# Kernel tuning notes

Measured on AMD Instinct MI355X. Metric: run time of the kernel, lower is better.

## Reference

```python
import jax, jax.numpy as jnp
import numpy as np

LN_EPS = 1e-5

def layer_norm(x, gamma, beta):
    mu = jnp.mean(x, axis=-1, keepdims=True)
    var = jnp.mean(jnp.square(x - mu), axis=-1, keepdims=True)
    return (x - mu) * jax.lax.rsqrt(var + LN_EPS) * gamma + beta

def setup_inputs() -> dict:
    key = jax.random.key(0)
    ks = jax.random.split(key, 10)
    B, C, N = 8, 256, 4096
    s = 1.0 / np.sqrt(C)
    inp = {
        "x": jax.random.normal(ks[0], (B, C, N), dtype=jnp.float32),
        "W_qkv": jax.random.uniform(ks[1], (C, C), jnp.float32, -s, s),            # Linear(dim, dim, bias=False)
        "W_mlp": jax.random.uniform(ks[2], (2 * C, 2 * C), jnp.float32, -0.5 * s, 0.5 * s),
        "b_mlp": jax.random.uniform(ks[3], (2 * C,), jnp.float32, -0.5 * s, 0.5 * s),
        "g1": jnp.ones((4 * C,), jnp.float32),
        "beta1": jnp.zeros((4 * C,), jnp.float32),
        "W_res": jax.random.uniform(ks[4], (C, 4 * C), jnp.float32, -0.25 * s, 0.25 * s),  # Linear(4*dim, dim, bias=False)
        "g2": jnp.ones((C,), jnp.float32),
        "beta2": jnp.zeros((C,), jnp.float32),
    }
    return inp

def reference(x, W_qkv, W_mlp, b_mlp, g1, beta1, W_res, g2, beta2):
    # x: (B, C, N) channels-first -> (B, N, C)
    NITER = 2  # niter_heads
    x = jnp.swapaxes(x, 1, 2)
    x = x @ W_qkv.T                                   # shared_qkv, (B, N, C)
    v = jax.lax.stop_gradient(x)                      # x.clone().detach()
    for _ in range(NITER):
        # first_context = x^T @ v : (B, C, C)
        ctx = jnp.einsum('bnc,bnd->bcd', x, v)
        out = jax.nn.softmax(x, axis=-1) @ ctx        # (B, N, C)
        cat1 = jnp.concatenate([out, v], axis=-1)     # (B, N, 2C)
        mlp = jax.nn.relu(cat1 @ W_mlp.T + b_mlp)     # (B, N, 2C)
        cat2 = jnp.concatenate([cat1, mlp], axis=-1)  # (B, N, 4C)
        # dropout layers are identity in eval mode
        v = layer_norm(cat2, g1, beta1) @ W_res.T + x # residual_mlp + skip
        v = layer_norm(x + v, g2, beta2)
    return jnp.swapaxes(v, 1, 2)                      # back to (B, C, N)
```

## Files before the change

### kernel.cpp

```cpp
#include <hip/hip_runtime.h>
#include <cstdint>
#include <cstddef>


using u16 = unsigned short;
using short8 = __attribute__((ext_vector_type(8))) short;
using bf16x8 = __attribute__((ext_vector_type(8))) __bf16;
using f32x4  = __attribute__((ext_vector_type(4))) float;
using i32x4  = __attribute__((ext_vector_type(4))) int;
using u16x4  = __attribute__((ext_vector_type(4))) u16;
using u16x8  = __attribute__((ext_vector_type(8))) u16;

__device__ __forceinline__ float b2f(u16 u) {
    union { unsigned u32; float f; } c; c.u32 = ((unsigned)u) << 16; return c.f;
}
__device__ __forceinline__ u16 f2b(float f) {
    union { float f; unsigned u; } c; c.f = f;
    unsigned r = c.u + 0x7FFFu + ((c.u >> 16) & 1u);
    return (u16)(r >> 16);
}
__device__ __forceinline__ void cvt(u16 a,  u16& o)   { o = a; }
__device__ __forceinline__ void cvt(float a, u16& o)  { o = f2b(a); }
__device__ __forceinline__ void cvt(float a, float& o){ o = a; }
__device__ __forceinline__ void cvt(u16 a,  float& o) { o = b2f(a); }

__device__ __forceinline__ void glds16(const u16* g, short* l) {
    __builtin_amdgcn_global_load_lds(
        (const __attribute__((address_space(1))) void*)g,
        (__attribute__((address_space(3))) void*)l, 16, 0, 0);
}

template<int MODE, int TRF>
__global__ __launch_bounds__(512)
void gemm_bt(const u16* __restrict__ A, const u16* __restrict__ A2,
             const u16* __restrict__ A3,
             int lda, int lda2, int lda3, int kSplit,
             const u16* __restrict__ B, int ldb, long strA, long strB,
             int statStride, int kChunk, int nKsplit,
             float* __restrict__ outF, u16* __restrict__ outB,
             long sOF, long sOB, int ldo,
             const u16* __restrict__ Xres,
             const float* __restrict__ bias,
             const float2* __restrict__ stats,
             const float* __restrict__ g, const float* __restrict__ be)
{
    __shared__ short lsA[128 * 64];
    __shared__ short lsB[128 * 64];

    const int bz    = blockIdx.z;
    const int batch = bz / nKsplit;
    const int ks    = bz - batch * nKsplit;
    const u16* Ab = A + (size_t)batch * strA;
    const u16* Bb = B + (size_t)batch * strB;
    const int colBase = blockIdx.x * 128;
    const int rowBase = blockIdx.y * 128;
    const int k0 = ks * kChunk;
    const int k1 = k0 + kChunk;

    const int t    = threadIdx.x;
    const int sRow = t >> 3;
    const int sKl  = (t & 7) << 3;
    const int sKg  = (((t & 7) ^ (sRow & 7)) << 3);

    const int lane = t & 63;
    const int w    = t >> 6;
    const int wr   = (w >> 1) * 32;
    const int wc   = (w & 1) * 64;
    const int mrow = lane & 15;
    const int q    = lane >> 4;

    short* ldA0 = &lsA[w * 512];
    short* ldA1 = &lsA[4096 + w * 512];
    short* ldB0 = &lsB[w * 512];
    short* ldB1 = &lsB[4096 + w * 512];

    float2 st0 = {0.f, 0.f}, st1 = {0.f, 0.f};
    if (TRF == 1) {
        const int sb = batch * statStride + rowBase;
        const float2 t0 = stats[sb + sRow];
        const float2 t1 = stats[sb + sRow + 64];
        st0 = make_float2(0.f, 1.f / t0.y);
        st1 = make_float2(0.f, 1.f / t1.y);
    }

    auto aPtr = [&](int rloc, int kn) -> const u16* {
        const int arow = rowBase + rloc + sRow;
        if (TRF == 2) {
            if (kn < 256)      return A  + (size_t)arow * lda  + kn + sKg;
            else if (kn < 512) return A2 + (size_t)arow * lda2 + (kn - 256) + sKg;
            else               return A3 + (size_t)arow * lda3 + (kn - 512) + sKg;
        } else if (TRF == 3) {
            if (kn < kSplit)   return Ab + (size_t)arow * lda + kn + sKg;
            return A2 + (size_t)arow * lda2 + (kn - kSplit) + sKg;
        }
        return Ab + (size_t)arow * lda + kn + sKg;
    };
    auto loadX = [&](int rloc, int kn, float2 st) -> i32x4 {
        const int arow = rowBase + rloc + sRow;
        i32x4 raw = *(const i32x4*)(Ab + (size_t)arow * lda + kn + sKg);
        short8 h = __builtin_bit_cast(short8, raw);
        short8 o;
#pragma unroll
        for (int i = 0; i < 8; i++) {
            float v = b2f((u16)h[i]);
            v = __expf(v - st.x) * st.y;
            o[i] = (short)f2b(v);
        }
        return __builtin_bit_cast(i32x4, o);
    };

    const f32x4 fzero = {0.f, 0.f, 0.f, 0.f};
    f32x4 acc[2][4];
#pragma unroll
    for (int i = 0; i < 2; i++)
#pragma unroll
        for (int j = 0; j < 4; j++) acc[i][j] = fzero;

    const u16* pB0 = Bb + (size_t)(colBase + sRow) * ldb + sKg;
    const u16* pB1 = pB0 + (size_t)64 * ldb;
    const u16* pA0 = nullptr; const u16* pA1 = nullptr;
    if (TRF == 0) {
        pA0 = Ab + (size_t)(rowBase + sRow) * lda + sKg;
        pA1 = pA0 + (size_t)64 * lda;
    }

    const int rsw = mrow & 7;
    const int kc0 = (((0 * 4 + q) ^ rsw) << 3);
    const int kc1 = (((1 * 4 + q) ^ rsw) << 3);

    i32x4 a0, a1;
    if (TRF == 1) {
        a0 = loadX(0,  k0, st0);
        a1 = loadX(64, k0, st1);
    }

    for (int kk = k0; kk < k1; kk += 64) {
        if (TRF == 1) {
            *(i32x4*)&lsA[sRow * 64 + sKl]        = a0;
            *(i32x4*)&lsA[(sRow + 64) * 64 + sKl] = a1;
        } else if (TRF == 0) {
            glds16(pA0 + kk, ldA0);
            glds16(pA1 + kk, ldA1);
        } else {
            glds16(aPtr(0,  kk), ldA0);
            glds16(aPtr(64, kk), ldA1);
        }
        glds16(pB0 + kk, ldB0);
        glds16(pB1 + kk, ldB1);
        __syncthreads();
        const int kn = kk + 64;
        if (TRF == 1 && kn < k1) {
            a0 = loadX(0,  kn, st0);
            a1 = loadX(64, kn, st1);
        }
#pragma unroll
        for (int h = 0; h < 2; h++) {
            const int kc = h ? kc1 : kc0;
            bf16x8 af[2], bfr[4];
#pragma unroll
            for (int mi = 0; mi < 2; mi++)
                af[mi] = __builtin_bit_cast(bf16x8,
                    *(const short8*)&lsA[(wr + mi * 16 + mrow) * 64 + kc]);
#pragma unroll
            for (int ni = 0; ni < 4; ni++)
                bfr[ni] = __builtin_bit_cast(bf16x8,
                    *(const short8*)&lsB[(wc + ni * 16 + mrow) * 64 + kc]);
#pragma unroll
            for (int mi = 0; mi < 2; mi++)
#pragma unroll
                for (int ni = 0; ni < 4; ni++)
                    acc[mi][ni] = __builtin_amdgcn_mfma_f32_16x16x32_bf16(
                        af[mi], bfr[ni], acc[mi][ni], 0, 0, 0);
        }
        __syncthreads();
    }

    if (MODE == 5) {
        u16* XT = const_cast<u16*>(Xres);
        float2* sm = const_cast<float2*>(stats);
        float rsum[2][4] = {{0.f,0.f,0.f,0.f},{0.f,0.f,0.f,0.f}};
#pragma unroll
        for (int mi = 0; mi < 2; mi++) {
#pragma unroll
            for (int ni = 0; ni < 4; ni++) {
                const int col  = colBase + wc + ni * 16 + mrow;
                const int row0 = rowBase + wr + mi * 16 + q * 4;
                u16x4 hv;
#pragma unroll
                for (int r = 0; r < 4; r++) {
                    const u16 h = f2b(acc[mi][ni][r]);
                    hv[r] = h;
                    outB[(size_t)(row0 + r) * ldo + col] = h;
                    rsum[mi][r] += __expf(b2f(h));
                }
                *(u16x4*)(XT + (size_t)(row0 >> 12) * 1048576
                             + (size_t)col * 4096 + (row0 & 4095)) = hv;
            }
        }
#pragma unroll
        for (int mi = 0; mi < 2; mi++)
#pragma unroll
            for (int r = 0; r < 4; r++) {
                float s = rsum[mi][r];
                s += __shfl_xor(s, 1); s += __shfl_xor(s, 2);
                s += __shfl_xor(s, 4); s += __shfl_xor(s, 8);
                if (mrow == 0)
                    atomicAdd(&sm[rowBase + wr + mi * 16 + q * 4 + r].y, s);
            }
        return;
    }

#pragma unroll
    for (int mi = 0; mi < 2; mi++) {
#pragma unroll
        for (int ni = 0; ni < 4; ni++) {
            const int col = colBase + wc + ni * 16 + mrow;
#pragma unroll
            for (int r = 0; r < 4; r++) {
                const int row = rowBase + wr + mi * 16 + q * 4 + r;
                float v = acc[mi][ni][r];
                if (MODE == 0) {
                    outB[(size_t)batch * sOB + (size_t)row * ldo + col] = f2b(v);
                } else if (MODE == 1) {
                    outF[((size_t)batch * nKsplit + ks) * sOF
                         + (size_t)row * ldo + col] = v;
                } else if (MODE == 3) {
                    v += bias[col];
                    v = v > 0.f ? v : 0.f;
                    outB[(size_t)row * ldo + col] = f2b(v);
                } else if (MODE == 4) {
                    const float2 ln = stats[row];
                    v = ln.y * (v - ln.x * g[col]) + be[col]
                        + 2.f * b2f(Xres[(size_t)row * 256 + col]);
                    outB[(size_t)row * ldo + col] = f2b(v);
                }
            }
        }
    }
}

template<typename TIN, typename TOUT>
__global__ __launch_bounds__(256)
void transpose_k(const TIN* __restrict__ in, TOUT* __restrict__ out,
                 int R, int Cc, long sIn, long sOut)
{
    __shared__ TOUT tile[32][33];
    const int b = blockIdx.z;
    const TIN* ib = in + (size_t)b * sIn;
    TOUT* ob = out + (size_t)b * sOut;
    const int c0 = blockIdx.x * 32, r0 = blockIdx.y * 32;
    const int tx = threadIdx.x & 31, ty = threadIdx.x >> 5;
#pragma unroll
    for (int i = 0; i < 32; i += 8)
        cvt(ib[(size_t)(r0 + ty + i) * Cc + c0 + tx], tile[ty + i][tx]);
    __syncthreads();
#pragma unroll
    for (int i = 0; i < 32; i += 8)
        ob[(size_t)(c0 + ty + i) * R + r0 + tx] = tile[tx][ty + i];
}

__global__ __launch_bounds__(256)
void zerosm_k(float2* __restrict__ p)
{
    p[blockIdx.x * 256 + threadIdx.x] = make_float2(0.f, 0.f);
}

__global__ __launch_bounds__(256)
void stats1024_k(const u16* __restrict__ OUT, const u16* __restrict__ V,
                 const u16* __restrict__ MLPo, float2* __restrict__ st)
{
    const int wave = threadIdx.x >> 6, lane = threadIdx.x & 63;
    const size_t row = (size_t)blockIdx.x * 4 + wave;
    const int c = lane * 16;
    const u16* src;
    if (c < 256)       src = OUT  + row * 256 + c;
    else if (c < 512)  src = V    + row * 256 + (c - 256);
    else               src = MLPo + row * 512 + (c - 512);
    short8 r0 = *(const short8*)(src);
    short8 r1 = *(const short8*)(src + 8);
    float s = 0.f, s2 = 0.f;
#pragma unroll
    for (int i = 0; i < 8; i++) {
        const float a = b2f((u16)r0[i]), b = b2f((u16)r1[i]);
        s += a + b; s2 += a * a + b * b;
    }
    for (int o = 32; o > 0; o >>= 1) { s += __shfl_xor(s, o); s2 += __shfl_xor(s2, o); }
    const float mean = s * (1.f / 1024.f);
    const float var  = s2 * (1.f / 1024.f) - mean * mean;
    if (lane == 0) st[row] = make_float2(mean, rsqrtf(var + 1e-5f));
}

template<typename OUTT, bool WRITE_VB>
__global__ __launch_bounds__(256)
void ln256t_k(const u16* __restrict__ Tb, const float* __restrict__ g,
              const float* __restrict__ be, u16* __restrict__ Vb,
              OUTT* __restrict__ outT)
{
    constexpr int STRIDE = (sizeof(OUTT) == 2) ? 266 : 261;
    __shared__ OUTT tile[32 * STRIDE];
    const int wid = threadIdx.x >> 6, lane = threadIdx.x & 63;
    const int bx = blockIdx.x;
    const size_t r0 = (size_t)bx * 32;
    const int b  = bx >> 7;
    const int n0 = (bx & 127) * 32;

#pragma unroll
    for (int j = 0; j < 8; j++) {
        const int lr = wid * 8 + j;
        const size_t row = r0 + lr;
        const u16x4 tb = *(const u16x4*)(Tb + row * 256 + lane * 4);
        const float x0 = b2f(tb.x), x1 = b2f(tb.y), x2 = b2f(tb.z), x3 = b2f(tb.w);
        float s  = x0 + x1 + x2 + x3;
        float s2 = x0 * x0 + x1 * x1 + x2 * x2 + x3 * x3;
        for (int o = 32; o > 0; o >>= 1) { s += __shfl_xor(s, o); s2 += __shfl_xor(s2, o); }
        const float mean = s * (1.f / 256.f);
        const float var  = s2 * (1.f / 256.f) - mean * mean;
        const float rstd = rsqrtf(var + 1e-5f);
        const int c = lane * 4;
        float4 ov = { (x0 - mean) * rstd * g[c + 0] + be[c + 0],
                      (x1 - mean) * rstd * g[c + 1] + be[c + 1],
                      (x2 - mean) * rstd * g[c + 2] + be[c + 2],
                      (x3 - mean) * rstd * g[c + 3] + be[c + 3] };
        if (WRITE_VB) {
            u16x4 vb = { f2b(ov.x), f2b(ov.y), f2b(ov.z), f2b(ov.w) };
            *(u16x4*)(Vb + row * 256 + c) = vb;
        }
        OUTT* tl = &tile[lr * STRIDE + c];
        cvt(ov.x, tl[0]); cvt(ov.y, tl[1]); cvt(ov.z, tl[2]); cvt(ov.w, tl[3]);
    }
    __syncthreads();

    const int c = threadIdx.x;
    OUTT* dst = outT + ((size_t)b * 256 + c) * 4096 + n0;
    if (sizeof(OUTT) == 2) {
#pragma unroll
        for (int k = 0; k < 4; k++) {
            u16x8 v;
#pragma unroll
            for (int i = 0; i < 8; i++) v[i] = *(const u16*)&tile[(k * 8 + i) * STRIDE + c];
            *(u16x8*)((u16*)dst + k * 8) = v;
        }
    } else {
#pragma unroll
        for (int k = 0; k < 8; k++) {
            float4 v;
            v.x = *(const float*)&tile[(k * 4 + 0) * STRIDE + c];
            v.y = *(const float*)&tile[(k * 4 + 1) * STRIDE + c];
            v.z = *(const float*)&tile[(k * 4 + 2) * STRIDE + c];
            v.w = *(const float*)&tile[(k * 4 + 3) * STRIDE + c];
            *(float4*)((float*)dst + k * 4) = v;
        }
    }
}

__global__ __launch_bounds__(256)
void ctxreduce_k(const float* __restrict__ ctxp, u16* __restrict__ ctxb)
{
    const int i = blockIdx.x * 256 + threadIdx.x;
    const int batch  = i >> 14;
    const int within = i & 16383;
    const float4* src = (const float4*)ctxp + (size_t)batch * 16 * 16384 + within;
    float4 s = {0.f, 0.f, 0.f, 0.f};
#pragma unroll
    for (int ks = 0; ks < 16; ks++) {
        const float4 v = src[(size_t)ks * 16384];
        s.x += v.x; s.y += v.y; s.z += v.z; s.w += v.w;
    }
    u16x4 o = { f2b(s.x), f2b(s.y), f2b(s.z), f2b(s.w) };
    ((u16x4*)ctxb)[i] = o;
}

__global__ __launch_bounds__(256)
void wconv_k(const float* __restrict__ Wq, const float* __restrict__ Wm,
             u16* __restrict__ oq, u16* __restrict__ om)
{
    const int i = blockIdx.x * 256 + threadIdx.x;
    const float* src; u16* dst; int j;
    if (i < 16384) { src = Wq; dst = oq; j = i; }
    else           { src = Wm; dst = om; j = i - 16384; }
    const float4 v = ((const float4*)src)[j];
    u16x4 o = { f2b(v.x), f2b(v.y), f2b(v.z), f2b(v.w) };
    ((u16x4*)dst)[j] = o;
}

__global__ __launch_bounds__(256)
void wresprep_k(const float* __restrict__ Wres, const float* __restrict__ g1,
                const float* __restrict__ be1, u16* __restrict__ Wr_b,
                float* __restrict__ sg, float* __restrict__ br)
{
    const int wv = threadIdx.x >> 6, lane = threadIdx.x & 63;
    const int row = blockIdx.x * 4 + wv;
    const float* src = Wres + (size_t)row * 1024;
    float s = 0.f, b = 0.f;
#pragma unroll
    for (int j = 0; j < 4; j++) {
        const int c = j * 256 + lane * 4;
        const float4 w  = *(const float4*)(src + c);
        const float4 gg = *(const float4*)(g1 + c);
        const float4 bb = *(const float4*)(be1 + c);
        const float4 wg = { w.x * gg.x, w.y * gg.y, w.z * gg.z, w.w * gg.w };
        u16x4 o = { f2b(wg.x), f2b(wg.y), f2b(wg.z), f2b(wg.w) };
        *(u16x4*)(Wr_b + (size_t)row * 1024 + c) = o;
        s += wg.x + wg.y + wg.z + wg.w;
        b += w.x * bb.x + w.y * bb.y + w.z * bb.z + w.w * bb.w;
    }
    for (int o = 32; o > 0; o >>= 1) { s += __shfl_xor(s, o); b += __shfl_xor(b, o); }
    if (lane == 0) { sg[row] = s; br[row] = b; }
}

extern "C" void kernel_launch(void* const* d_in, const int* in_sizes, int n_in,
                              void* d_out, int out_size, void* d_ws, size_t ws_size,
                              hipStream_t stream)
{
    (void)in_sizes; (void)n_in; (void)out_size; (void)ws_size;
    const float* x    = (const float*)d_in[0];
    const float* Wqkv = (const float*)d_in[1];
    const float* Wmlp = (const float*)d_in[2];
    const float* bmlp = (const float*)d_in[3];
    const float* g1   = (const float*)d_in[4];
    const float* be1  = (const float*)d_in[5];
    const float* Wres = (const float*)d_in[6];
    const float* g2   = (const float*)d_in[7];
    const float* be2  = (const float*)d_in[8];

    char* ws = (char*)d_ws;
    u16*    Xb   = (u16*)ws;    ws += (size_t)16777216;
    u16*    XT   = (u16*)ws;    ws += (size_t)16777216;
    u16*    Vb   = (u16*)ws;    ws += (size_t)16777216;
    u16*    VT2  = (u16*)ws;    ws += (size_t)16777216;
    u16*    OUT  = (u16*)ws;    ws += (size_t)16777216;
    u16*    MLPo = (u16*)ws;    ws += (size_t)33554432;
    u16*    Tb   = (u16*)ws;    ws += (size_t)16777216;
    float*  ctxp = (float*)ws;  ws += (size_t)33554432;
    u16*    ctxb = (u16*)ws;    ws += (size_t)1048576;
    float2* smst = (float2*)ws; ws += (size_t)262144;
    float2* lnst = (float2*)ws; ws += (size_t)262144;
    u16*    Wq_b = (u16*)ws;    ws += (size_t)131072;
    u16*    Wm_b = (u16*)ws;    ws += (size_t)524288;
    u16*    Wr_b = (u16*)ws;    ws += (size_t)524288;
    float*  sg   = (float*)ws;  ws += (size_t)1024;
    float*  br   = (float*)ws;  ws += (size_t)1024;
    u16*    xt   = MLPo;

    wconv_k<<<dim3(320), 256, 0, stream>>>(Wqkv, Wmlp, Wq_b, Wm_b);
    wresprep_k<<<dim3(64), 256, 0, stream>>>(Wres, g1, be1, Wr_b, sg, br);
    zerosm_k<<<dim3(128), 256, 0, stream>>>(smst);

    transpose_k<float, u16><<<dim3(128, 8, 8), 256, 0, stream>>>(
        x, xt, 256, 4096, 256L * 4096, 4096L * 256);

    gemm_bt<5, 0><<<dim3(2, 256, 1), 512, 0, stream>>>(
        xt, nullptr, nullptr, 256, 0, 0, 0, Wq_b, 256, 0, 0, 0, 256, 1,
        nullptr, Xb, 0, 0, 256, XT, nullptr, smst, nullptr, nullptr);

    const u16* VTcur = XT;
    const u16* Vcur  = Xb;

    for (int it = 0; it < 2; ++it) {
        gemm_bt<1, 0><<<dim3(2, 2, 128), 512, 0, stream>>>(
            VTcur, nullptr, nullptr, 4096, 0, 0, 0, XT, 4096,
            1048576, 1048576, 0, 256, 16,
            ctxp, nullptr, 65536, 0, 256, nullptr, nullptr, nullptr, nullptr, nullptr);
        ctxreduce_k<<<dim3(512), 256, 0, stream>>>(ctxp, ctxb);

        gemm_bt<0, 1><<<dim3(2, 32, 8), 512, 0, stream>>>(
            Xb, nullptr, nullptr, 256, 0, 0, 0, ctxb, 256,
            1048576, 65536, 4096, 256, 1,
            nullptr, OUT, 0, 1048576, 256, nullptr, nullptr, smst, nullptr, nullptr);

        gemm_bt<3, 3><<<dim3(4, 256, 1), 512, 0, stream>>>(
            OUT, Vcur, nullptr, 256, 256, 0, 256, Wm_b, 512, 0, 0, 0, 512, 1,
            nullptr, MLPo, 0, 0, 512, nullptr, bmlp, nullptr, nullptr, nullptr);

        stats1024_k<<<dim3(8192), 256, 0, stream>>>(OUT, Vcur, MLPo, lnst);

        gemm_bt<4, 2><<<dim3(2, 256, 1), 512, 0, stream>>>(
            OUT, Vcur, MLPo, 256, 256, 512, 0, Wr_b, 1024, 0, 0, 0, 1024, 1,
            nullptr, Tb, 0, 0, 256, Xb, nullptr, lnst, sg, br);

        if (it == 0) {
            ln256t_k<u16, true><<<dim3(1024), 256, 0, stream>>>(
                Tb, g2, be2, Vb, VT2);
            VTcur = VT2;
            Vcur  = Vb;
        } else {
            ln256t_k<float, false><<<dim3(1024), 256, 0, stream>>>(
                Tb, g2, be2, nullptr, (float*)d_out);
        }
    }
}
```

Baseline: 355.4 us.

## Fuse LayerNorm-1024 statistics into GEMM epilogues and precompute softmax operand

Drops the separate stats1024 pass that re-read OUT, V and MLP outputs. Row sum and sum-of-squares are now accumulated with atomics in the out-GEMM and MLP-GEMM epilogues, V stats come from the LN256 kernel or a new pre-pass, and the residual GEMM derives mean and rstd itself. Softmax(x) is also materialised once as a bf16 buffer so the out-GEMM uses a plain epilogue. The cost is extra atomics, a zeroing step folded into ctxreduce, and an extra 16 MB buffer plus one pre-pass kernel.

```diff
diff --git a/kernel.cpp b/kernel.cpp
--- a/kernel.cpp
+++ b/kernel.cpp
@@ -210,6 +210,85 @@
         return;
     }
 
+    if (MODE == 6 || MODE == 7) {
+        float2* om = const_cast<float2*>(stats);
+        float ss[2][4]  = {{0.f,0.f,0.f,0.f},{0.f,0.f,0.f,0.f}};
+        float ss2[2][4] = {{0.f,0.f,0.f,0.f},{0.f,0.f,0.f,0.f}};
+#pragma unroll
+        for (int mi = 0; mi < 2; mi++) {
+#pragma unroll
+            for (int ni = 0; ni < 4; ni++) {
+                const int col = colBase + wc + ni * 16 + mrow;
+#pragma unroll
+                for (int r = 0; r < 4; r++) {
+                    const int row = rowBase + wr + mi * 16 + q * 4 + r;
+                    float v = acc[mi][ni][r];
+                    if (MODE == 7) {
+                        v += bias[col];
+                        v = v > 0.f ? v : 0.f;
+                    }
+                    const u16 h = f2b(v);
+                    outB[(size_t)batch * sOB + (size_t)row * ldo + col] = h;
+                    const float uf = b2f(h);
+                    ss[mi][r]  += uf;
+                    ss2[mi][r] += uf * uf;
+                }
+            }
+        }
+#pragma unroll
+        for (int mi = 0; mi < 2; mi++)
+#pragma unroll
+            for (int r = 0; r < 4; r++) {
+                float s  = ss[mi][r], s2 = ss2[mi][r];
+                s  += __shfl_xor(s, 1);  s  += __shfl_xor(s, 2);
+                s  += __shfl_xor(s, 4);  s  += __shfl_xor(s, 8);
+                s2 += __shfl_xor(s2, 1); s2 += __shfl_xor(s2, 2);
+                s2 += __shfl_xor(s2, 4); s2 += __shfl_xor(s2, 8);
+                if (mrow == 0) {
+                    const int grow = batch * statStride
+                                   + rowBase + wr + mi * 16 + q * 4 + r;
+                    atomicAdd(&om[grow].x, s);
+                    atomicAdd(&om[grow].y, s2);
+                }
+            }
+        return;
+    }
+
+    if (MODE == 4) {
+        const float2* om = (const float2*)bias;
+        float mean_[2][4], rstd_[2][4];
+#pragma unroll
+        for (int mi = 0; mi < 2; mi++)
+#pragma unroll
+            for (int r = 0; r < 4; r++) {
+                const int row = rowBase + wr + mi * 16 + q * 4 + r;
+                const float2 vs = stats[row];
+                const float2 os = om[row];
+                const float s  = vs.x + os.x;
+                const float s2 = vs.y + os.y;
+                const float mean = s * (1.f / 1024.f);
+                const float var  = s2 * (1.f / 1024.f) - mean * mean;
+                mean_[mi][r] = mean;
+                rstd_[mi][r] = rsqrtf(var + 1e-5f);
+            }
+#pragma unroll
+        for (int mi = 0; mi < 2; mi++) {
+#pragma unroll
+            for (int ni = 0; ni < 4; ni++) {
+                const int col = colBase + wc + ni * 16 + mrow;
+#pragma unroll
+                for (int r = 0; r < 4; r++) {
+                    const int row = rowBase + wr + mi * 16 + q * 4 + r;
+                    float v = acc[mi][ni][r];
+                    v = rstd_[mi][r] * (v - mean_[mi][r] * g[col]) + be[col]
+                        + 2.f * b2f(Xres[(size_t)row * 256 + col]);
+                    outB[(size_t)row * ldo + col] = f2b(v);
+                }
+            }
+        }
+        return;
+    }
+
 #pragma unroll
     for (int mi = 0; mi < 2; mi++) {
 #pragma unroll
@@ -228,11 +307,6 @@
                     v += bias[col];
                     v = v > 0.f ? v : 0.f;
                     outB[(size_t)row * ldo + col] = f2b(v);
-                } else if (MODE == 4) {
-                    const float2 ln = stats[row];
-                    v = ln.y * (v - ln.x * g[col]) + be[col]
-                        + 2.f * b2f(Xres[(size_t)row * 256 + col]);
-                    outB[(size_t)row * ldo + col] = f2b(v);
                 }
             }
         }
@@ -266,35 +340,28 @@
 }
 
 __global__ __launch_bounds__(256)
-void stats1024_k(const u16* __restrict__ OUT, const u16* __restrict__ V,
-                 const u16* __restrict__ MLPo, float2* __restrict__ st)
+void sxb_k(const u16* __restrict__ Xb, const float2* __restrict__ smst,
+           u16* __restrict__ SXb, float2* __restrict__ vstat)
 {
     const int wave = threadIdx.x >> 6, lane = threadIdx.x & 63;
     const size_t row = (size_t)blockIdx.x * 4 + wave;
-    const int c = lane * 16;
-    const u16* src;
-    if (c < 256)       src = OUT  + row * 256 + c;
-    else if (c < 512)  src = V    + row * 256 + (c - 256);
-    else               src = MLPo + row * 512 + (c - 512);
-    short8 r0 = *(const short8*)(src);
-    short8 r1 = *(const short8*)(src + 8);
-    float s = 0.f, s2 = 0.f;
-#pragma unroll
-    for (int i = 0; i < 8; i++) {
-        const float a = b2f((u16)r0[i]), b = b2f((u16)r1[i]);
-        s += a + b; s2 += a * a + b * b;
-    }
-    for (int o = 32; o > 0; o >>= 1) { s += __shfl_xor(s, o); s2 += __shfl_xor(s2, o); }
-    const float mean = s * (1.f / 1024.f);
-    const float var  = s2 * (1.f / 1024.f) - mean * mean;
-    if (lane == 0) st[row] = make_float2(mean, rsqrtf(var + 1e-5f));
+    const u16x4 xb = *(const u16x4*)(Xb + row * 256 + lane * 4);
+    const float rs = 1.f / smst[row].y;
+    const float x0 = b2f(xb.x), x1 = b2f(xb.y), x2 = b2f(xb.z), x3 = b2f(xb.w);
+    u16x4 o = { f2b(__expf(x0) * rs), f2b(__expf(x1) * rs),
+                f2b(__expf(x2) * rs), f2b(__expf(x3) * rs) };
+    *(u16x4*)(SXb + row * 256 + lane * 4) = o;
+    float s  = x0 + x1 + x2 + x3;
+    float s2 = x0 * x0 + x1 * x1 + x2 * x2 + x3 * x3;
+    for (int d = 32; d > 0; d >>= 1) { s += __shfl_xor(s, d); s2 += __shfl_xor(s2, d); }
+    if (lane == 0) vstat[row] = make_float2(s, s2);
 }
 
 template<typename OUTT, bool WRITE_VB>
 __global__ __launch_bounds__(256)
 void ln256t_k(const u16* __restrict__ Tb, const float* __restrict__ g,
               const float* __restrict__ be, u16* __restrict__ Vb,
-              OUTT* __restrict__ outT)
+              OUTT* __restrict__ outT, float2* __restrict__ vstat)
 {
     constexpr int STRIDE = (sizeof(OUTT) == 2) ? 266 : 261;
     __shared__ OUTT tile[32 * STRIDE];
@@ -324,6 +391,12 @@
         if (WRITE_VB) {
             u16x4 vb = { f2b(ov.x), f2b(ov.y), f2b(ov.z), f2b(ov.w) };
             *(u16x4*)(Vb + row * 256 + c) = vb;
+            const float u0 = b2f(vb.x), u1 = b2f(vb.y),
+                        u2 = b2f(vb.z), u3 = b2f(vb.w);
+            float vs  = u0 + u1 + u2 + u3;
+            float vs2 = u0 * u0 + u1 * u1 + u2 * u2 + u3 * u3;
+            for (int o = 32; o > 0; o >>= 1) { vs += __shfl_xor(vs, o); vs2 += __shfl_xor(vs2, o); }
+            if (lane == 0) vstat[row] = make_float2(vs, vs2);
         }
         OUTT* tl = &tile[lr * STRIDE + c];
         cvt(ov.x, tl[0]); cvt(ov.y, tl[1]); cvt(ov.z, tl[2]); cvt(ov.w, tl[3]);
@@ -354,9 +427,11 @@
 }
 
 __global__ __launch_bounds__(256)
-void ctxreduce_k(const float* __restrict__ ctxp, u16* __restrict__ ctxb)
+void ctxreduce_k(const float* __restrict__ ctxp, u16* __restrict__ ctxb,
+                 float2* __restrict__ om)
 {
     const int i = blockIdx.x * 256 + threadIdx.x;
+    if (i < 32768) om[i] = make_float2(0.f, 0.f);
     const int batch  = i >> 14;
     const int within = i & 16383;
     const float4* src = (const float4*)ctxp + (size_t)batch * 16 * 16384 + within;
@@ -426,6 +501,7 @@
     char* ws = (char*)d_ws;
     u16*    Xb   = (u16*)ws;    ws += (size_t)16777216;
     u16*    XT   = (u16*)ws;    ws += (size_t)16777216;
+    u16*    SXb  = (u16*)ws;    ws += (size_t)16777216;
     u16*    Vb   = (u16*)ws;    ws += (size_t)16777216;
     u16*    VT2  = (u16*)ws;    ws += (size_t)16777216;
     u16*    OUT  = (u16*)ws;    ws += (size_t)16777216;
@@ -434,7 +510,8 @@
     float*  ctxp = (float*)ws;  ws += (size_t)33554432;
     u16*    ctxb = (u16*)ws;    ws += (size_t)1048576;
     float2* smst = (float2*)ws; ws += (size_t)262144;
-    float2* lnst = (float2*)ws; ws += (size_t)262144;
+    float2* vstat= (float2*)ws; ws += (size_t)262144;
+    float2* omst = (float2*)ws; ws += (size_t)262144;
     u16*    Wq_b = (u16*)ws;    ws += (size_t)131072;
     u16*    Wm_b = (u16*)ws;    ws += (size_t)524288;
     u16*    Wr_b = (u16*)ws;    ws += (size_t)524288;
@@ -453,6 +530,8 @@
         xt, nullptr, nullptr, 256, 0, 0, 0, Wq_b, 256, 0, 0, 0, 256, 1,
         nullptr, Xb, 0, 0, 256, XT, nullptr, smst, nullptr, nullptr);
 
+    sxb_k<<<dim3(8192), 256, 0, stream>>>(Xb, smst, SXb, vstat);
+
     const u16* VTcur = XT;
     const u16* Vcur  = Xb;
 
@@ -461,31 +540,29 @@
             VTcur, nullptr, nullptr, 4096, 0, 0, 0, XT, 4096,
             1048576, 1048576, 0, 256, 16,
             ctxp, nullptr, 65536, 0, 256, nullptr, nullptr, nullptr, nullptr, nullptr);
-        ctxreduce_k<<<dim3(512), 256, 0, stream>>>(ctxp, ctxb);
-
-        gemm_bt<0, 1><<<dim3(2, 32, 8), 512, 0, stream>>>(
-            Xb, nullptr, nullptr, 256, 0, 0, 0, ctxb, 256,
+        ctxreduce_k<<<dim3(512), 256, 0, stream>>>(ctxp, ctxb, omst);
+
+        gemm_bt<6, 0><<<dim3(2, 32, 8), 512, 0, stream>>>(
+            SXb, nullptr, nullptr, 256, 0, 0, 0, ctxb, 256,
             1048576, 65536, 4096, 256, 1,
-            nullptr, OUT, 0, 1048576, 256, nullptr, nullptr, smst, nullptr, nullptr);
-
-        gemm_bt<3, 3><<<dim3(4, 256, 1), 512, 0, stream>>>(
+            nullptr, OUT, 0, 1048576, 256, nullptr, nullptr, omst, nullptr, nullptr);
+
+        gemm_bt<7, 3><<<dim3(4, 256, 1), 512, 0, stream>>>(
             OUT, Vcur, nullptr, 256, 256, 0, 256, Wm_b, 512, 0, 0, 0, 512, 1,
-            nullptr, MLPo, 0, 0, 512, nullptr, bmlp, nullptr, nullptr, nullptr);
-
-        stats1024_k<<<dim3(8192), 256, 0, stream>>>(OUT, Vcur, MLPo, lnst);
+            nullptr, MLPo, 0, 0, 512, nullptr, bmlp, omst, nullptr, nullptr);
 
         gemm_bt<4, 2><<<dim3(2, 256, 1), 512, 0, stream>>>(
             OUT, Vcur, MLPo, 256, 256, 512, 0, Wr_b, 1024, 0, 0, 0, 1024, 1,
-            nullptr, Tb, 0, 0, 256, Xb, nullptr, lnst, sg, br);
+            nullptr, Tb, 0, 0, 256, Xb, (const float*)omst, vstat, sg, br);
 
         if (it == 0) {
             ln256t_k<u16, true><<<dim3(1024), 256, 0, stream>>>(
-                Tb, g2, be2, Vb, VT2);
+                Tb, g2, be2, Vb, VT2, vstat);
             VTcur = VT2;
             Vcur  = Vb;
         } else {
             ln256t_k<float, false><<<dim3(1024), 256, 0, stream>>>(
-                Tb, g2, be2, nullptr, (float*)d_out);
-        }
-    }
-}
+                Tb, g2, be2, nullptr, (float*)d_out, nullptr);
+        }
+    }
+}
```

Measured after the change: 372.6 us. +4.9%, slower.
